# Kernel tuning notes

Measured on AMD Instinct MI355X. Metric: run time of the kernel, lower is better.

## Reference

```python
import jax, jax.numpy as jnp
import numpy as np

GROUPS = 32
EPS = 1e-6


def setup_inputs() -> dict:
    key = jax.random.key(0)
    ks = jax.random.split(key, 6)
    B, C, H, W = 2, 512, 64, 64
    s = 1.0 / np.sqrt(C)
    return {
        "x": jax.random.normal(ks[0], (B, C, H, W), dtype=jnp.float32),
        "gn_scale": jnp.ones((C,), dtype=jnp.float32),
        "gn_bias": jnp.zeros((C,), dtype=jnp.float32),
        "wq": jax.random.normal(ks[1], (C, C), dtype=jnp.float32) * s,
        "bq": jnp.zeros((C,), dtype=jnp.float32),
        "wk": jax.random.normal(ks[2], (C, C), dtype=jnp.float32) * s,
        "bk": jnp.zeros((C,), dtype=jnp.float32),
        "wv": jax.random.normal(ks[3], (C, C), dtype=jnp.float32) * s,
        "bv": jnp.zeros((C,), dtype=jnp.float32),
        "wp": jax.random.normal(ks[4], (C, C), dtype=jnp.float32) * s,
        "bp": jnp.zeros((C,), dtype=jnp.float32),
    }


def reference(x, gn_scale, gn_bias, wq, bq, wk, bk, wv, bv, wp, bp):
    B, C, H, W = x.shape
    N = H * W
    # GroupNorm(32, C, eps=1e-6) with affine, over (channels-per-group, H, W)
    g = x.reshape(B, GROUPS, C // GROUPS, N)
    mean = jnp.mean(g, axis=(2, 3), keepdims=True)
    var = jnp.var(g, axis=(2, 3), keepdims=True)
    h = ((g - mean) * jax.lax.rsqrt(var + EPS)).reshape(B, C, N)
    h = h * gn_scale[None, :, None] + gn_bias[None, :, None]
    # 1x1 convs == channel-wise linear maps; h is [B, C, N]
    q = jnp.einsum('oc,bcn->bon', wq, h) + bq[None, :, None]
    k = jnp.einsum('oc,bcn->bon', wk, h) + bk[None, :, None]
    v = jnp.einsum('oc,bcn->bon', wv, h) + bv[None, :, None]
    # full attention (chunking in original is a tiling detail; same math)
    scores = jnp.einsum('bci,bcj->bij', q, k) * (C ** -0.5)  # [B, N, N]
    attn = jax.nn.softmax(scores, axis=-1)
    out = jnp.einsum('bij,bcj->bci', attn, v)  # [B, C, N]
    hp = jnp.einsum('oc,bcn->bon', wp, out) + bp[None, :, None]
    return x + hp.reshape(B, C, H, W)
```

## Files before the change

kernel.cpp:

```cpp
#include <hip/hip_runtime.h>
#include <math.h>

#define BB 2
#define CC_ 512
#define GG 32
#define CG 16
#define NN 4096
#define NCH 4
#define EPSF 1e-6f
#define SCALEF 0.04419417382415922f

typedef unsigned short ushort_t;
typedef __bf16 bf16x8 __attribute__((ext_vector_type(8)));
typedef ushort_t ushortx8 __attribute__((ext_vector_type(8)));
typedef float floatx4 __attribute__((ext_vector_type(4)));

__device__ __forceinline__ ushort_t f2bf(float f) {
    union { float f; unsigned u; } x; x.f = f;
    unsigned r = (x.u + 0x7FFFu + ((x.u >> 16) & 1u)) >> 16;
    return (ushort_t)r;
}
__device__ __forceinline__ float bf2f(ushort_t v) {
    union { unsigned u; float f; } x; x.u = ((unsigned)v) << 16; return x.f;
}

__global__ __launch_bounds__(256) void wprep(const float* __restrict__ wq,
                                             const float* __restrict__ wk,
                                             const float* __restrict__ wv,
                                             const float* __restrict__ wp,
                                             ushort_t* __restrict__ wqkv,
                                             ushort_t* __restrict__ wpb) {
    int idx4 = blockIdx.x * 256 + threadIdx.x;
    int m = idx4 >> 16;
    int r = idx4 & 65535;
    const float* src = (m == 0) ? wq : (m == 1) ? wk : (m == 2) ? wv : wp;
    float4 v = ((const float4*)src)[r];
    ushort4 u;
    u.x = f2bf(v.x); u.y = f2bf(v.y); u.z = f2bf(v.z); u.w = f2bf(v.w);
    if (m < 3) ((ushort4*)wqkv)[(size_t)m * 65536 + r] = u;
    else       ((ushort4*)wpb)[r] = u;
}

__global__ __launch_bounds__(256) void gn_stats(const float* __restrict__ x,
                                                float* __restrict__ mv) {
    int bg = blockIdx.x;
    const float4* xp = (const float4*)(x + (size_t)bg * (CG * NN));
    float s = 0.f, ss = 0.f;
    for (int idx = threadIdx.x; idx < CG * NN / 4; idx += 256) {
        float4 v = xp[idx];
        s  += (v.x + v.y) + (v.z + v.w);
        ss += v.x * v.x + v.y * v.y + v.z * v.z + v.w * v.w;
    }
    __shared__ float sm[8];
    for (int off = 32; off > 0; off >>= 1) {
        s  += __shfl_down(s, off, 64);
        ss += __shfl_down(ss, off, 64);
    }
    int lane = threadIdx.x & 63, wv = threadIdx.x >> 6;
    if (lane == 0) { sm[wv] = s; sm[4 + wv] = ss; }
    __syncthreads();
    if (threadIdx.x == 0) {
        s  = sm[0] + sm[1] + sm[2] + sm[3];
        ss = sm[4] + sm[5] + sm[6] + sm[7];
        const float inv = 1.0f / (float)(CG * NN);
        float mean = s * inv;
        float var  = ss * inv - mean * mean;
        mv[bg]      = mean;
        mv[64 + bg] = rsqrtf(var + EPSF);
    }
}

__global__ __launch_bounds__(256) void gn_apply_t(const float* __restrict__ x,
                                                  const float* __restrict__ gamma,
                                                  const float* __restrict__ beta,
                                                  const float* __restrict__ mv,
                                                  ushort_t* __restrict__ hT) {
    const int b  = blockIdx.z;
    const int c0 = blockIdx.y * 64;
    const int n0 = blockIdx.x * 64;
    __shared__ float T[64][65];
    const int tid = threadIdx.x;
#pragma unroll
    for (int it = 0; it < 4; ++it) {
        int c  = it * 16 + (tid >> 4);
        int n4 = (tid & 15) * 4;
        int bg = b * 32 + ((c0 + c) >> 4);
        float a  = mv[64 + bg] * gamma[c0 + c];
        float b2 = beta[c0 + c] - mv[bg] * a;
        float4 v = *(const float4*)&x[((size_t)b * CC_ + c0 + c) * NN + n0 + n4];
        T[c][n4 + 0] = v.x * a + b2;
        T[c][n4 + 1] = v.y * a + b2;
        T[c][n4 + 2] = v.z * a + b2;
        T[c][n4 + 3] = v.w * a + b2;
    }
    __syncthreads();
#pragma unroll
    for (int it = 0; it < 4; ++it) {
        int n  = it * 16 + (tid >> 4);
        int c4 = (tid & 15) * 4;
        ushort4 u;
        u.x = f2bf(T[c4 + 0][n]); u.y = f2bf(T[c4 + 1][n]);
        u.z = f2bf(T[c4 + 2][n]); u.w = f2bf(T[c4 + 3][n]);
        *(ushort4*)&hT[((size_t)b * NN + n0 + n) * CC_ + c0 + c4] = u;
    }
}

__global__ __launch_bounds__(256) void conv_qkv(const ushort_t* __restrict__ hT,
                                                const ushort_t* __restrict__ wqkv,
                                                const float* __restrict__ bq,
                                                const float* __restrict__ bk,
                                                const float* __restrict__ bv,
                                                ushort_t* __restrict__ qT,
                                                ushort_t* __restrict__ kT,
                                                ushort_t* __restrict__ vB) {
    constexpr int ASTR = 40;
    __shared__ __align__(16) char smem[34816];
    ushort_t* At = (ushort_t*)smem;
    ushort_t* Bt = At + 128 * ASTR;

    const int m0  = blockIdx.x * 128;
    const int o0g = blockIdx.y * 128;
    const int matid = o0g >> 9;
    const int o0 = o0g & 511;
    const int tid = threadIdx.x;
    const int w = tid >> 6, lane = tid & 63, quad = lane >> 4, n16 = lane & 15;
    const int wm = w & 1, wn = w >> 1;
    const int r2 = tid >> 1, half = tid & 1;

    floatx4 acc[4][4];
#pragma unroll
    for (int i = 0; i < 4; ++i)
#pragma unroll
        for (int j = 0; j < 4; ++j) acc[i][j] = (floatx4){0.f, 0.f, 0.f, 0.f};

    for (int k0 = 0; k0 < CC_; k0 += 32) {
        const ushort_t* asrc = &hT[(size_t)(m0 + r2) * CC_ + k0 + half * 16];
        bf16x8 a0 = *(const bf16x8*)(asrc);
        bf16x8 a1 = *(const bf16x8*)(asrc + 8);
        const ushort_t* wsrc = &wqkv[(size_t)(o0g + r2) * CC_ + k0 + half * 16];
        bf16x8 w0 = *(const bf16x8*)(wsrc);
        bf16x8 w1 = *(const bf16x8*)(wsrc + 8);
        __syncthreads();
        *(bf16x8*)&At[r2 * ASTR + half * 16]     = a0;
        *(bf16x8*)&At[r2 * ASTR + half * 16 + 8] = a1;
        *(bf16x8*)&Bt[r2 * ASTR + half * 16]     = w0;
        *(bf16x8*)&Bt[r2 * ASTR + half * 16 + 8] = w1;
        __syncthreads();
        bf16x8 af[4], bf_[4];
#pragma unroll
        for (int mt = 0; mt < 4; ++mt)
            af[mt] = *(const bf16x8*)&At[(wm * 64 + mt * 16 + n16) * ASTR + quad * 8];
#pragma unroll
        for (int nt = 0; nt < 4; ++nt)
            bf_[nt] = *(const bf16x8*)&Bt[(wn * 64 + nt * 16 + n16) * ASTR + quad * 8];
#pragma unroll
        for (int mt = 0; mt < 4; ++mt)
#pragma unroll
            for (int nt = 0; nt < 4; ++nt)
                acc[mt][nt] = __builtin_amdgcn_mfma_f32_16x16x32_bf16(af[mt], bf_[nt], acc[mt][nt], 0, 0, 0);
    }

    const float* bias = (matid == 0) ? bq : (matid == 1) ? bk : bv;
    float bsv[4];
#pragma unroll
    for (int nt = 0; nt < 4; ++nt) bsv[nt] = bias[o0 + wn * 64 + nt * 16 + n16];

    if (matid < 2) {
        float scale = (matid == 0) ? SCALEF : 1.0f;
        ushort_t* dst = (matid == 0) ? qT : kT;
#pragma unroll
        for (int mt = 0; mt < 4; ++mt)
#pragma unroll
            for (int nt = 0; nt < 4; ++nt) {
                int o = o0 + wn * 64 + nt * 16 + n16;
#pragma unroll
                for (int r = 0; r < 4; ++r) {
                    int m = m0 + wm * 64 + mt * 16 + quad * 4 + r;
                    dst[(size_t)m * CC_ + o] = f2bf((acc[mt][nt][r] + bsv[nt]) * scale);
                }
            }
    } else {
        __syncthreads();
        ushort_t* T = (ushort_t*)smem;
#pragma unroll
        for (int mt = 0; mt < 4; ++mt)
#pragma unroll
            for (int nt = 0; nt < 4; ++nt) {
                int ol = wn * 64 + nt * 16 + n16;
#pragma unroll
                for (int r = 0; r < 4; ++r) {
                    int nl = wm * 64 + mt * 16 + quad * 4 + r;
                    T[ol * 136 + nl] = f2bf(acc[mt][nt][r] + bsv[nt]);
                }
            }
        __syncthreads();
        const int bb = m0 >> 12;
        const int n0 = m0 & (NN - 1);
#pragma unroll
        for (int i = 0; i < 8; ++i) {
            ushortx8 v = *(const ushortx8*)&T[r2 * 136 + half * 64 + i * 8];
            *(ushortx8*)&vB[((size_t)bb * CC_ + o0 + r2) * NN + n0 + half * 64 + i * 8] = v;
        }
    }
}

__global__ __launch_bounds__(512, 2) void flash_attn5(
        const ushort_t* __restrict__ qT, const ushort_t* __restrict__ kT,
        const ushort_t* __restrict__ vB,
        ushort_t* __restrict__ opart, float* __restrict__ lpart) {
    const int b     = blockIdx.z;
    const int chunk = blockIdx.y;
    const int i0    = blockIdx.x * 128;
    const ushort_t* qTb = qT + (size_t)b * NN * CC_;
    const ushort_t* kTb = kT + (size_t)b * NN * CC_;
    const ushort_t* vBb = vB + (size_t)b * CC_ * NN;

    __shared__ ushort_t Klds[2][64 * 520];
    __shared__ ushort_t Plds[128 * 72];

    const int tid  = threadIdx.x;
    const int w    = tid >> 6;
    const int lane = tid & 63;
    const int quad = lane >> 4;
    const int n16  = lane & 15;
    const int cb   = w * 64;

    bf16x8 aq[16];
    {
        const ushort_t* qrow = qTb + (size_t)(i0 + w * 16 + n16) * CC_ + quad * 8;
#pragma unroll
        for (int ks = 0; ks < 16; ++ks) aq[ks] = *(const bf16x8*)(qrow + ks * 32);
    }

    floatx4 acc[8][4];
#pragma unroll
    for (int mt = 0; mt < 8; ++mt)
#pragma unroll
        for (int st = 0; st < 4; ++st) acc[mt][st] = (floatx4){0.f, 0.f, 0.f, 0.f};
    float lsum[4] = {0.f, 0.f, 0.f, 0.f};

    const int jbase = chunk * (NN / NCH);
    constexpr int NT = (NN / NCH) / 64;

#pragma unroll
    for (int it = 0; it < 8; ++it) {
        int row = w * 8 + it;
        __builtin_amdgcn_global_load_lds(
            (const __attribute__((address_space(1))) unsigned int*)
                (kTb + (size_t)(jbase + row) * CC_ + lane * 8),
            (__attribute__((address_space(3))) unsigned int*)(&Klds[0][row * 520]),
            16, 0, 0);
    }

    for (int t = 0; t < NT; ++t) {
        const int j0 = jbase + t * 64;
        const ushort_t* Kbuf = Klds[t & 1];
        __syncthreads();

        bf16x8 bv0[4], bv1[4];
#pragma unroll
        for (int st = 0; st < 4; ++st) {
            const ushort_t* vp = vBb + (size_t)(cb + st * 16 + n16) * NN + j0 + quad * 8;
            bv0[st] = *(const bf16x8*)(vp);
            bv1[st] = *(const bf16x8*)(vp + 32);
        }

#pragma unroll
        for (int js = 0; js < 4; ++js) {
            floatx4 s = (floatx4){0.f, 0.f, 0.f, 0.f};
            const ushort_t* kb = &Kbuf[(js * 16 + n16) * 520 + quad * 8];
#pragma unroll
            for (int ks = 0; ks < 16; ++ks) {
                bf16x8 bk = *(const bf16x8*)(kb + ks * 32);
                s = __builtin_amdgcn_mfma_f32_16x16x32_bf16(aq[ks], bk, s, 0, 0, 0);
            }
            float e0 = __expf(s[0]), e1 = __expf(s[1]);
            float e2 = __expf(s[2]), e3 = __expf(s[3]);
            lsum[0] += e0; lsum[1] += e1; lsum[2] += e2; lsum[3] += e3;
            const int pr = w * 16 + quad * 4;
            Plds[(pr + 0) * 72 + js * 16 + n16] = f2bf(e0);
            Plds[(pr + 1) * 72 + js * 16 + n16] = f2bf(e1);
            Plds[(pr + 2) * 72 + js * 16 + n16] = f2bf(e2);
            Plds[(pr + 3) * 72 + js * 16 + n16] = f2bf(e3);
        }
        __syncthreads();

        if (t + 1 < NT) {
#pragma unroll
            for (int it = 0; it < 8; ++it) {
                int row = w * 8 + it;
                __builtin_amdgcn_global_load_lds(
                    (const __attribute__((address_space(1))) unsigned int*)
                        (kTb + (size_t)(j0 + 64 + row) * CC_ + lane * 8),
                    (__attribute__((address_space(3))) unsigned int*)
                        (&Klds[(t + 1) & 1][row * 520]),
                    16, 0, 0);
            }
        }

#pragma unroll
        for (int mt = 0; mt < 8; ++mt) {
            const ushort_t* pr = &Plds[(mt * 16 + n16) * 72 + quad * 8];
            bf16x8 ap0 = *(const bf16x8*)(pr);
            bf16x8 ap1 = *(const bf16x8*)(pr + 32);
#pragma unroll
            for (int st = 0; st < 4; ++st) {
                acc[mt][st] = __builtin_amdgcn_mfma_f32_16x16x32_bf16(ap0, bv0[st], acc[mt][st], 0, 0, 0);
                acc[mt][st] = __builtin_amdgcn_mfma_f32_16x16x32_bf16(ap1, bv1[st], acc[mt][st], 0, 0, 0);
            }
        }
    }

#pragma unroll
    for (int r = 0; r < 4; ++r) {
        float p = lsum[r];
        p += __shfl_xor(p, 1);
        p += __shfl_xor(p, 2);
        p += __shfl_xor(p, 4);
        p += __shfl_xor(p, 8);
        lsum[r] = p;
    }

    if (n16 == 0) {
        float* lp = lpart + ((size_t)b * NCH + chunk) * NN + i0 + w * 16 + quad * 4;
        lp[0] = lsum[0]; lp[1] = lsum[1]; lp[2] = lsum[2]; lp[3] = lsum[3];
    }
    ushort_t* opb = opart + ((size_t)b * NCH + chunk) * CC_ * NN;
#pragma unroll
    for (int mt = 0; mt < 8; ++mt)
#pragma unroll
        for (int st = 0; st < 4; ++st) {
            int c = cb + st * 16 + n16;
            int n = i0 + mt * 16 + quad * 4;
            ushort4 u;
            u.x = f2bf(acc[mt][st][0]); u.y = f2bf(acc[mt][st][1]);
            u.z = f2bf(acc[mt][st][2]); u.w = f2bf(acc[mt][st][3]);
            *(ushort4*)&opb[(size_t)c * NN + n] = u;
        }
}

__global__ __launch_bounds__(256) void combine(const ushort_t* __restrict__ opart,
                                               const float* __restrict__ lpart,
                                               ushort_t* __restrict__ attnT) {
    const int b  = blockIdx.z;
    const int c0 = blockIdx.y * 64;
    const int n0 = blockIdx.x * 64;
    __shared__ float S[64][65];
    const int tid = threadIdx.x;
#pragma unroll
    for (int it = 0; it < 4; ++it) {
        int c  = it * 16 + (tid >> 4);
        int n4 = (tid & 15) * 4;
        float s0 = 0.f, s1 = 0.f, s2 = 0.f, s3 = 0.f;
#pragma unroll
        for (int k = 0; k < NCH; ++k) {
            ushort4 u = *(const ushort4*)&opart[(((size_t)b * NCH + k) * CC_ + c0 + c) * NN + n0 + n4];
            s0 += bf2f(u.x); s1 += bf2f(u.y); s2 += bf2f(u.z); s3 += bf2f(u.w);
        }
        S[c][n4 + 0] = s0; S[c][n4 + 1] = s1; S[c][n4 + 2] = s2; S[c][n4 + 3] = s3;
    }
    __syncthreads();
#pragma unroll
    for (int it = 0; it < 4; ++it) {
        int n  = it * 16 + (tid >> 4);
        int c4 = (tid & 15) * 4;
        float l = 0.f;
#pragma unroll
        for (int k = 0; k < NCH; ++k) l += lpart[((size_t)b * NCH + k) * NN + n0 + n];
        float linv = 1.0f / l;
        ushort4 u;
        u.x = f2bf(S[c4 + 0][n] * linv); u.y = f2bf(S[c4 + 1][n] * linv);
        u.z = f2bf(S[c4 + 2][n] * linv); u.w = f2bf(S[c4 + 3][n] * linv);
        *(ushort4*)&attnT[((size_t)b * NN + n0 + n) * CC_ + c0 + c4] = u;
    }
}

__global__ __launch_bounds__(256) void conv_proj(const ushort_t* __restrict__ attnT,
                                                 const ushort_t* __restrict__ wpb,
                                                 const float* __restrict__ bp,
                                                 const float* __restrict__ x,
                                                 float* __restrict__ out) {
    constexpr int ASTR = 40;
    __shared__ __align__(16) char smem[33792];
    ushort_t* At = (ushort_t*)smem;
    ushort_t* Bt = At + 128 * ASTR;

    const int m0 = blockIdx.x * 128;
    const int o0 = blockIdx.y * 64;
    const int tid = threadIdx.x;
    const int w = tid >> 6, lane = tid & 63, quad = lane >> 4, n16 = lane & 15;
    const int wm = w & 1, wn = w >> 1;
    const int r2 = tid >> 1, half = tid & 1;

    floatx4 acc[4][2];
#pragma unroll
    for (int i = 0; i < 4; ++i)
#pragma unroll
        for (int j = 0; j < 2; ++j) acc[i][j] = (floatx4){0.f, 0.f, 0.f, 0.f};

    for (int k0 = 0; k0 < CC_; k0 += 32) {
        const ushort_t* asrc = &attnT[(size_t)(m0 + r2) * CC_ + k0 + half * 16];
        bf16x8 a0 = *(const bf16x8*)(asrc);
        bf16x8 a1 = *(const bf16x8*)(asrc + 8);
        bf16x8 w0, w1;
        if (tid < 128) {
            const ushort_t* wsrc = &wpb[(size_t)(o0 + r2) * CC_ + k0 + half * 16];
            w0 = *(const bf16x8*)(wsrc);
            w1 = *(const bf16x8*)(wsrc + 8);
        }
        __syncthreads();
        *(bf16x8*)&At[r2 * ASTR + half * 16]     = a0;
        *(bf16x8*)&At[r2 * ASTR + half * 16 + 8] = a1;
        if (tid < 128) {
            *(bf16x8*)&Bt[r2 * ASTR + half * 16]     = w0;
            *(bf16x8*)&Bt[r2 * ASTR + half * 16 + 8] = w1;
        }
        __syncthreads();
        bf16x8 af[4], bf_[2];
#pragma unroll
        for (int mt = 0; mt < 4; ++mt)
            af[mt] = *(const bf16x8*)&At[(wm * 64 + mt * 16 + n16) * ASTR + quad * 8];
#pragma unroll
        for (int nt = 0; nt < 2; ++nt)
            bf_[nt] = *(const bf16x8*)&Bt[(wn * 32 + nt * 16 + n16) * ASTR + quad * 8];
#pragma unroll
        for (int mt = 0; mt < 4; ++mt)
#pragma unroll
            for (int nt = 0; nt < 2; ++nt)
                acc[mt][nt] = __builtin_amdgcn_mfma_f32_16x16x32_bf16(af[mt], bf_[nt], acc[mt][nt], 0, 0, 0);
    }

    float bsv[2];
#pragma unroll
    for (int nt = 0; nt < 2; ++nt) bsv[nt] = bp[o0 + wn * 32 + nt * 16 + n16];

    __syncthreads();
    float* Tf = (float*)smem;
#pragma unroll
    for (int mt = 0; mt < 4; ++mt)
#pragma unroll
        for (int nt = 0; nt < 2; ++nt) {
            int ol = wn * 32 + nt * 16 + n16;
#pragma unroll
            for (int r = 0; r < 4; ++r) {
                int nl = wm * 64 + mt * 16 + quad * 4 + r;
                Tf[ol * 132 + nl] = acc[mt][nt][r] + bsv[nt];
            }
        }
    __syncthreads();
    const int bb = m0 >> 12;
    const int n0 = m0 & (NN - 1);
    const int ro = tid >> 2;
    const int cc = (tid & 3) * 32;
    const size_t obase = ((size_t)bb * CC_ + o0 + ro) * NN + n0 + cc;
#pragma unroll
    for (int i = 0; i < 8; ++i) {
        float4 v  = *(const float4*)&Tf[ro * 132 + cc + i * 4];
        float4 x4 = *(const float4*)&x[obase + i * 4];
        v.x += x4.x; v.y += x4.y; v.z += x4.z; v.w += x4.w;
        *(float4*)&out[obase + i * 4] = v;
    }
}

extern "C" void kernel_launch(void* const* d_in, const int* in_sizes, int n_in,
                              void* d_out, int out_size, void* d_ws, size_t ws_size,
                              hipStream_t stream) {
    const float* x        = (const float*)d_in[0];
    const float* gn_scale = (const float*)d_in[1];
    const float* gn_bias  = (const float*)d_in[2];
    const float* wq = (const float*)d_in[3];
    const float* bq = (const float*)d_in[4];
    const float* wk = (const float*)d_in[5];
    const float* bk = (const float*)d_in[6];
    const float* wv = (const float*)d_in[7];
    const float* bv = (const float*)d_in[8];
    const float* wp = (const float*)d_in[9];
    const float* bp = (const float*)d_in[10];
    float* outp = (float*)d_out;

    const size_t TENS = (size_t)BB * CC_ * NN;
    ushort_t* hT    = (ushort_t*)d_ws;
    ushort_t* qT    = hT    + TENS;
    ushort_t* kT    = qT    + TENS;
    ushort_t* vB    = kT    + TENS;
    ushort_t* attnT = vB    + TENS;
    ushort_t* opart = attnT + TENS;
    ushort_t* wqkv  = opart + (size_t)NCH * TENS;
    ushort_t* wpb   = wqkv  + (size_t)1536 * 512;
    float*    lpart = (float*)(wpb + (size_t)512 * 512);
    float*    mv    = lpart + (size_t)BB * NCH * NN;

    wprep<<<1024, 256, 0, stream>>>(wq, wk, wv, wp, wqkv, wpb);
    gn_stats<<<BB * GG, 256, 0, stream>>>(x, mv);
    gn_apply_t<<<dim3(NN / 64, CC_ / 64, BB), 256, 0, stream>>>(x, gn_scale, gn_bias, mv, hT);

    conv_qkv<<<dim3(BB * NN / 128, 1536 / 128), 256, 0, stream>>>(
        hT, wqkv, bq, bk, bv, qT, kT, vB);

    flash_attn5<<<dim3(NN / 128, NCH, BB), 512, 0, stream>>>(qT, kT, vB, opart, lpart);
    combine<<<dim3(NN / 64, CC_ / 64, BB), 256, 0, stream>>>(opart, lpart, attnT);

    conv_proj<<<dim3(BB * NN / 128, CC_ / 64), 256, 0, stream>>>(attnT, wpb, bp, x, outp);
}
```

Baseline: 288.6 us.

## Software-pipeline flash attention PV one tile behind and widen conv K-steps

The attention kernel now uses 32-key tiles with a double-buffered P tile in shared memory. The P·V product for the previous tile runs while the current tile's QK scores are computed, and the K prefetch for the next tile is issued at the top of each iteration. This removes one barrier per tile and overlaps V loads and PV MFMAs with QK work, but it doubles the number of iterations and barriers. Both 1x1-conv GEMMs now stage 64-wide K slices per barrier pair instead of 32, halving their synchronization count at the cost of more shared memory.

```diff
diff --git a/kernel.cpp b/kernel.cpp
--- a/kernel.cpp
+++ b/kernel.cpp
@@ -113,8 +113,8 @@
                                                 ushort_t* __restrict__ qT,
                                                 ushort_t* __restrict__ kT,
                                                 ushort_t* __restrict__ vB) {
-    constexpr int ASTR = 40;
-    __shared__ __align__(16) char smem[34816];
+    constexpr int ASTR = 72;
+    __shared__ __align__(16) char smem[36864];
     ushort_t* At = (ushort_t*)smem;
     ushort_t* Bt = At + 128 * ASTR;
 
@@ -133,31 +133,42 @@
 #pragma unroll
         for (int j = 0; j < 4; ++j) acc[i][j] = (floatx4){0.f, 0.f, 0.f, 0.f};
 
-    for (int k0 = 0; k0 < CC_; k0 += 32) {
-        const ushort_t* asrc = &hT[(size_t)(m0 + r2) * CC_ + k0 + half * 16];
+    for (int k0 = 0; k0 < CC_; k0 += 64) {
+        const ushort_t* asrc = &hT[(size_t)(m0 + r2) * CC_ + k0 + half * 32];
         bf16x8 a0 = *(const bf16x8*)(asrc);
         bf16x8 a1 = *(const bf16x8*)(asrc + 8);
-        const ushort_t* wsrc = &wqkv[(size_t)(o0g + r2) * CC_ + k0 + half * 16];
+        bf16x8 a2 = *(const bf16x8*)(asrc + 16);
+        bf16x8 a3 = *(const bf16x8*)(asrc + 24);
+        const ushort_t* wsrc = &wqkv[(size_t)(o0g + r2) * CC_ + k0 + half * 32];
         bf16x8 w0 = *(const bf16x8*)(wsrc);
         bf16x8 w1 = *(const bf16x8*)(wsrc + 8);
-        __syncthreads();
-        *(bf16x8*)&At[r2 * ASTR + half * 16]     = a0;
-        *(bf16x8*)&At[r2 * ASTR + half * 16 + 8] = a1;
-        *(bf16x8*)&Bt[r2 * ASTR + half * 16]     = w0;
-        *(bf16x8*)&Bt[r2 * ASTR + half * 16 + 8] = w1;
-        __syncthreads();
-        bf16x8 af[4], bf_[4];
-#pragma unroll
-        for (int mt = 0; mt < 4; ++mt)
-            af[mt] = *(const bf16x8*)&At[(wm * 64 + mt * 16 + n16) * ASTR + quad * 8];
-#pragma unroll
-        for (int nt = 0; nt < 4; ++nt)
-            bf_[nt] = *(const bf16x8*)&Bt[(wn * 64 + nt * 16 + n16) * ASTR + quad * 8];
-#pragma unroll
-        for (int mt = 0; mt < 4; ++mt)
+        bf16x8 w2 = *(const bf16x8*)(wsrc + 16);
+        bf16x8 w3 = *(const bf16x8*)(wsrc + 24);
+        __syncthreads();
+        {
+            ushort_t* ad = &At[r2 * ASTR + half * 32];
+            *(bf16x8*)(ad)      = a0; *(bf16x8*)(ad + 8)  = a1;
+            *(bf16x8*)(ad + 16) = a2; *(bf16x8*)(ad + 24) = a3;
+            ushort_t* bd = &Bt[r2 * ASTR + half * 32];
+            *(bf16x8*)(bd)      = w0; *(bf16x8*)(bd + 8)  = w1;
+            *(bf16x8*)(bd + 16) = w2; *(bf16x8*)(bd + 24) = w3;
+        }
+        __syncthreads();
+#pragma unroll
+        for (int ks2 = 0; ks2 < 2; ++ks2) {
+            bf16x8 af[4], bf_[4];
+#pragma unroll
+            for (int mt = 0; mt < 4; ++mt)
+                af[mt] = *(const bf16x8*)&At[(wm * 64 + mt * 16 + n16) * ASTR + ks2 * 32 + quad * 8];
 #pragma unroll
             for (int nt = 0; nt < 4; ++nt)
-                acc[mt][nt] = __builtin_amdgcn_mfma_f32_16x16x32_bf16(af[mt], bf_[nt], acc[mt][nt], 0, 0, 0);
+                bf_[nt] = *(const bf16x8*)&Bt[(wn * 64 + nt * 16 + n16) * ASTR + ks2 * 32 + quad * 8];
+#pragma unroll
+            for (int mt = 0; mt < 4; ++mt)
+#pragma unroll
+                for (int nt = 0; nt < 4; ++nt)
+                    acc[mt][nt] = __builtin_amdgcn_mfma_f32_16x16x32_bf16(af[mt], bf_[nt], acc[mt][nt], 0, 0, 0);
+        }
     }
 
     const float* bias = (matid == 0) ? bq : (matid == 1) ? bk : bv;
@@ -204,7 +215,7 @@
     }
 }
 
-__global__ __launch_bounds__(512, 2) void flash_attn5(
+__global__ __launch_bounds__(512, 2) void flash_attn6(
         const ushort_t* __restrict__ qT, const ushort_t* __restrict__ kT,
         const ushort_t* __restrict__ vB,
         ushort_t* __restrict__ opart, float* __restrict__ lpart) {
@@ -215,8 +226,8 @@
     const ushort_t* kTb = kT + (size_t)b * NN * CC_;
     const ushort_t* vBb = vB + (size_t)b * CC_ * NN;
 
-    __shared__ ushort_t Klds[2][64 * 520];
-    __shared__ ushort_t Plds[128 * 72];
+    __shared__ ushort_t Klds[2][32 * 520];
+    __shared__ ushort_t Plds[2][128 * 40];
 
     const int tid  = threadIdx.x;
     const int w    = tid >> 6;
@@ -240,33 +251,47 @@
     float lsum[4] = {0.f, 0.f, 0.f, 0.f};
 
     const int jbase = chunk * (NN / NCH);
-    constexpr int NT = (NN / NCH) / 64;
-
-#pragma unroll
-    for (int it = 0; it < 8; ++it) {
-        int row = w * 8 + it;
+    constexpr int NT = (NN / NCH) / 32;
+
+#pragma unroll
+    for (int it = 0; it < 4; ++it) {
+        int row = w * 4 + it;
         __builtin_amdgcn_global_load_lds(
             (const __attribute__((address_space(1))) unsigned int*)
                 (kTb + (size_t)(jbase + row) * CC_ + lane * 8),
             (__attribute__((address_space(3))) unsigned int*)(&Klds[0][row * 520]),
             16, 0, 0);
     }
+    __syncthreads();
 
     for (int t = 0; t < NT; ++t) {
-        const int j0 = jbase + t * 64;
         const ushort_t* Kbuf = Klds[t & 1];
-        __syncthreads();
-
-        bf16x8 bv0[4], bv1[4];
-#pragma unroll
-        for (int st = 0; st < 4; ++st) {
-            const ushort_t* vp = vBb + (size_t)(cb + st * 16 + n16) * NN + j0 + quad * 8;
-            bv0[st] = *(const bf16x8*)(vp);
-            bv1[st] = *(const bf16x8*)(vp + 32);
-        }
-
-#pragma unroll
-        for (int js = 0; js < 4; ++js) {
+        ushort_t*       Pcur = Plds[t & 1];
+
+        if (t + 1 < NT) {
+            const int jn = jbase + (t + 1) * 32;
+#pragma unroll
+            for (int it = 0; it < 4; ++it) {
+                int row = w * 4 + it;
+                __builtin_amdgcn_global_load_lds(
+                    (const __attribute__((address_space(1))) unsigned int*)
+                        (kTb + (size_t)(jn + row) * CC_ + lane * 8),
+                    (__attribute__((address_space(3))) unsigned int*)
+                        (&Klds[(t + 1) & 1][row * 520]),
+                    16, 0, 0);
+            }
+        }
+
+        bf16x8 bv[4];
+        if (t > 0) {
+            const int jp = jbase + (t - 1) * 32;
+#pragma unroll
+            for (int st = 0; st < 4; ++st)
+                bv[st] = *(const bf16x8*)(vBb + (size_t)(cb + st * 16 + n16) * NN + jp + quad * 8);
+        }
+
+#pragma unroll
+        for (int js = 0; js < 2; ++js) {
             floatx4 s = (floatx4){0.f, 0.f, 0.f, 0.f};
             const ushort_t* kb = &Kbuf[(js * 16 + n16) * 520 + quad * 8];
 #pragma unroll
@@ -278,36 +303,39 @@
             float e2 = __expf(s[2]), e3 = __expf(s[3]);
             lsum[0] += e0; lsum[1] += e1; lsum[2] += e2; lsum[3] += e3;
             const int pr = w * 16 + quad * 4;
-            Plds[(pr + 0) * 72 + js * 16 + n16] = f2bf(e0);
-            Plds[(pr + 1) * 72 + js * 16 + n16] = f2bf(e1);
-            Plds[(pr + 2) * 72 + js * 16 + n16] = f2bf(e2);
-            Plds[(pr + 3) * 72 + js * 16 + n16] = f2bf(e3);
-        }
-        __syncthreads();
-
-        if (t + 1 < NT) {
-#pragma unroll
-            for (int it = 0; it < 8; ++it) {
-                int row = w * 8 + it;
-                __builtin_amdgcn_global_load_lds(
-                    (const __attribute__((address_space(1))) unsigned int*)
-                        (kTb + (size_t)(j0 + 64 + row) * CC_ + lane * 8),
-                    (__attribute__((address_space(3))) unsigned int*)
-                        (&Klds[(t + 1) & 1][row * 520]),
-                    16, 0, 0);
-            }
-        }
-
+            Pcur[(pr + 0) * 40 + js * 16 + n16] = f2bf(e0);
+            Pcur[(pr + 1) * 40 + js * 16 + n16] = f2bf(e1);
+            Pcur[(pr + 2) * 40 + js * 16 + n16] = f2bf(e2);
+            Pcur[(pr + 3) * 40 + js * 16 + n16] = f2bf(e3);
+        }
+
+        if (t > 0) {
+            const ushort_t* Pprev = Plds[(t - 1) & 1];
+#pragma unroll
+            for (int mt = 0; mt < 8; ++mt) {
+                bf16x8 ap = *(const bf16x8*)&Pprev[(mt * 16 + n16) * 40 + quad * 8];
+#pragma unroll
+                for (int st = 0; st < 4; ++st)
+                    acc[mt][st] = __builtin_amdgcn_mfma_f32_16x16x32_bf16(ap, bv[st], acc[mt][st], 0, 0, 0);
+            }
+        }
+
+        __syncthreads();
+    }
+
+    {
+        const int jp = jbase + (NT - 1) * 32;
+        bf16x8 bv[4];
+#pragma unroll
+        for (int st = 0; st < 4; ++st)
+            bv[st] = *(const bf16x8*)(vBb + (size_t)(cb + st * 16 + n16) * NN + jp + quad * 8);
+        const ushort_t* Pprev = Plds[(NT - 1) & 1];
 #pragma unroll
         for (int mt = 0; mt < 8; ++mt) {
-            const ushort_t* pr = &Plds[(mt * 16 + n16) * 72 + quad * 8];
-            bf16x8 ap0 = *(const bf16x8*)(pr);
-            bf16x8 ap1 = *(const bf16x8*)(pr + 32);
-#pragma unroll
-            for (int st = 0; st < 4; ++st) {
-                acc[mt][st] = __builtin_amdgcn_mfma_f32_16x16x32_bf16(ap0, bv0[st], acc[mt][st], 0, 0, 0);
-                acc[mt][st] = __builtin_amdgcn_mfma_f32_16x16x32_bf16(ap1, bv1[st], acc[mt][st], 0, 0, 0);
-            }
+            bf16x8 ap = *(const bf16x8*)&Pprev[(mt * 16 + n16) * 40 + quad * 8];
+#pragma unroll
+            for (int st = 0; st < 4; ++st)
+                acc[mt][st] = __builtin_amdgcn_mfma_f32_16x16x32_bf16(ap, bv[st], acc[mt][st], 0, 0, 0);
         }
     }
 
@@ -380,7 +408,7 @@
                                                  const float* __restrict__ bp,
                                                  const float* __restrict__ x,
                                                  float* __restrict__ out) {
-    constexpr int ASTR = 40;
+    constexpr int ASTR = 72;
     __shared__ __align__(16) char smem[33792];
     ushort_t* At = (ushort_t*)smem;
     ushort_t* Bt = At + 128 * ASTR;
@@ -398,36 +426,47 @@
 #pragma unroll
         for (int j = 0; j < 2; ++j) acc[i][j] = (floatx4){0.f, 0.f, 0.f, 0.f};
 
-    for (int k0 = 0; k0 < CC_; k0 += 32) {
-        const ushort_t* asrc = &attnT[(size_t)(m0 + r2) * CC_ + k0 + half * 16];
+    for (int k0 = 0; k0 < CC_; k0 += 64) {
+        const ushort_t* asrc = &attnT[(size_t)(m0 + r2) * CC_ + k0 + half * 32];
         bf16x8 a0 = *(const bf16x8*)(asrc);
         bf16x8 a1 = *(const bf16x8*)(asrc + 8);
-        bf16x8 w0, w1;
+        bf16x8 a2 = *(const bf16x8*)(asrc + 16);
+        bf16x8 a3 = *(const bf16x8*)(asrc + 24);
+        bf16x8 w0, w1, w2, w3;
         if (tid < 128) {
-            const ushort_t* wsrc = &wpb[(size_t)(o0 + r2) * CC_ + k0 + half * 16];
+            const ushort_t* wsrc = &wpb[(size_t)(o0 + r2) * CC_ + k0 + half * 32];
             w0 = *(const bf16x8*)(wsrc);
             w1 = *(const bf16x8*)(wsrc + 8);
-        }
-        __syncthreads();
-        *(bf16x8*)&At[r2 * ASTR + half * 16]     = a0;
-        *(bf16x8*)&At[r2 * ASTR + half * 16 + 8] = a1;
-        if (tid < 128) {
-            *(bf16x8*)&Bt[r2 * ASTR + half * 16]     = w0;
-            *(bf16x8*)&Bt[r2 * ASTR + half * 16 + 8] = w1;
-        }
-        __syncthreads();
-        bf16x8 af[4], bf_[2];
-#pragma unroll
-        for (int mt = 0; mt < 4; ++mt)
-            af[mt] = *(const bf16x8*)&At[(wm * 64 + mt * 16 + n16) * ASTR + quad * 8];
-#pragma unroll
-        for (int nt = 0; nt < 2; ++nt)
-            bf_[nt] = *(const bf16x8*)&Bt[(wn * 32 + nt * 16 + n16) * ASTR + quad * 8];
-#pragma unroll
-        for (int mt = 0; mt < 4; ++mt)
+            w2 = *(const bf16x8*)(wsrc + 16);
+            w3 = *(const bf16x8*)(wsrc + 24);
+        }
+        __syncthreads();
+        {
+            ushort_t* ad = &At[r2 * ASTR + half * 32];
+            *(bf16x8*)(ad)      = a0; *(bf16x8*)(ad + 8)  = a1;
+            *(bf16x8*)(ad + 16) = a2; *(bf16x8*)(ad + 24) = a3;
+            if (tid < 128) {
+                ushort_t* bd = &Bt[r2 * ASTR + half * 32];
+                *(bf16x8*)(bd)      = w0; *(bf16x8*)(bd + 8)  = w1;
+                *(bf16x8*)(bd + 16) = w2; *(bf16x8*)(bd + 24) = w3;
+            }
+        }
+        __syncthreads();
+#pragma unroll
+        for (int ks2 = 0; ks2 < 2; ++ks2) {
+            bf16x8 af[4], bf_[2];
+#pragma unroll
+            for (int mt = 0; mt < 4; ++mt)
+                af[mt] = *(const bf16x8*)&At[(wm * 64 + mt * 16 + n16) * ASTR + ks2 * 32 + quad * 8];
 #pragma unroll
             for (int nt = 0; nt < 2; ++nt)
-                acc[mt][nt] = __builtin_amdgcn_mfma_f32_16x16x32_bf16(af[mt], bf_[nt], acc[mt][nt], 0, 0, 0);
+                bf_[nt] = *(const bf16x8*)&Bt[(wn * 32 + nt * 16 + n16) * ASTR + ks2 * 32 + quad * 8];
+#pragma unroll
+            for (int mt = 0; mt < 4; ++mt)
+#pragma unroll
+                for (int nt = 0; nt < 2; ++nt)
+                    acc[mt][nt] = __builtin_amdgcn_mfma_f32_16x16x32_bf16(af[mt], bf_[nt], acc[mt][nt], 0, 0, 0);
+        }
     }
 
     float bsv[2];
@@ -497,7 +536,7 @@
     conv_qkv<<<dim3(BB * NN / 128, 1536 / 128), 256, 0, stream>>>(
         hT, wqkv, bq, bk, bv, qT, kT, vB);
 
-    flash_attn5<<<dim3(NN / 128, NCH, BB), 512, 0, stream>>>(qT, kT, vB, opart, lpart);
+    flash_attn6<<<dim3(NN / 128, NCH, BB), 512, 0, stream>>>(qT, kT, vB, opart, lpart);
     combine<<<dim3(NN / 64, CC_ / 64, BB), 256, 0, stream>>>(opart, lpart, attnT);
 
     conv_proj<<<dim3(BB * NN / 128, CC_ / 64), 256, 0, stream>>>(attnT, wpb, bp, x, outp);
```

Result: faster. 265.8 us (-7.9%).
